# Kernel optimization log

Measured on AMD Instinct MI355X. Metric: run time of the kernel, lower is better.

## Reference

```python
import jax, jax.numpy as jnp
import numpy as np

N_ENTS = 50000
N_RELS = 500
EMB = 256
N_LAYERS = 2
N_EDGES = 400000
BATCH = 512
BN_EPS = 1e-5


def make_quaternion_mul(kernel):
    # kernel: [m, 4*dim] -> hamilton: [4*m, 4*dim]
    r, i, j, k = jnp.split(kernel, 4, axis=1)
    r2 = jnp.concatenate([r, -i, -j, -k], axis=0)
    i2 = jnp.concatenate([i, r, -k, j], axis=0)
    j2 = jnp.concatenate([j, k, r, -i], axis=0)
    k2 = jnp.concatenate([k, -j, i, r], axis=0)
    return jnp.concatenate([r2, i2, j2, k2], axis=1)


def batchnorm(x, gamma, beta):
    mean = jnp.mean(x, axis=0)
    var = jnp.var(x, axis=0)  # biased, as torch BN training normalization
    return (x - mean) * jax.lax.rsqrt(var + BN_EPS) * gamma + beta


def q4gnn_layer(X, rows, cols, vals, W, gamma, beta, n_nodes):
    hamilton = make_quaternion_mul(W)          # [d, d]
    support = X @ hamilton                     # [n, d]
    agg = jax.ops.segment_sum(vals[:, None] * support[cols], rows, num_segments=n_nodes)
    return jnp.tanh(batchnorm(agg, gamma, beta))


def vec_vec_wise_multiplication(q, p):
    # quaternion componentwise-normalized hamilton product; q, p: [B, d]
    d = q.shape[1]
    size = d // 4
    pn = p.reshape(-1, 4, size)
    pn = pn / jnp.sqrt(jnp.sum(pn * pn, axis=1, keepdims=True))
    pn = pn.reshape(-1, d)
    qr, qi, qj, qk = jnp.split(q, 4, axis=1)
    q_r = jnp.concatenate([qr, -qi, -qj, -qk], axis=1)
    q_i = jnp.concatenate([qi, qr, -qk, qj], axis=1)
    q_j = jnp.concatenate([qj, qk, qr, -qi], axis=1)
    q_k = jnp.concatenate([qk, -qj, qi, qr], axis=1)
    def qwise(x):
        return jnp.sum((x * pn).reshape(-1, 4, size), axis=1)
    return jnp.concatenate([qwise(q_r), qwise(q_i), qwise(q_j), qwise(q_k)], axis=1)


def quate_score(h, r, X, gamma, beta):
    hr = vec_vec_wise_multiplication(h, r)
    hr = batchnorm(hr, gamma, beta)            # dropout = identity (eval)
    return hr @ X.T                            # [B, n_ents]


def setup_inputs() -> dict:
    key = jax.random.key(0)
    ks = jax.random.split(key, 12)
    return {
        "e1_idx": jax.random.randint(ks[0], (BATCH,), 0, N_ENTS),
        "r_idx": jax.random.randint(ks[1], (BATCH,), 0, N_RELS),
        "embeddings": jax.random.normal(ks[2], (N_ENTS + N_RELS, EMB), jnp.float32) * 0.1,
        "gcn1_w": jax.random.normal(ks[3], (N_LAYERS, EMB // 4, EMB), jnp.float32) * 0.1,
        "gcn2_w": jax.random.normal(ks[4], (N_LAYERS, EMB // 4, EMB), jnp.float32) * 0.1,
        "gcn1_gamma": jnp.ones((N_LAYERS, EMB), jnp.float32),
        "gcn1_beta": jnp.zeros((N_LAYERS, EMB), jnp.float32),
        "gcn2_gamma": jnp.ones((N_LAYERS, EMB), jnp.float32),
        "gcn2_beta": jnp.zeros((N_LAYERS, EMB), jnp.float32),
        "lin_ents": jax.random.normal(ks[5], (N_LAYERS, EMB // 2, EMB), jnp.float32) * 0.1,
        "bn_s_gamma": jnp.ones((3, EMB), jnp.float32),
        "bn_s_beta": jnp.zeros((3, EMB), jnp.float32),
        "adj_rows": jax.random.randint(ks[6], (N_EDGES,), 0, N_ENTS),
        "adj_cols": jax.random.randint(ks[7], (N_EDGES,), 0, N_ENTS),
        "adj_vals": jax.random.uniform(ks[8], (N_EDGES,), jnp.float32),
        "adjr_rows": jax.random.randint(ks[9], (N_EDGES,), 0, N_ENTS + N_RELS),
        "adjr_cols": jax.random.randint(ks[10], (N_EDGES,), 0, N_ENTS + N_RELS),
        "adjr_vals": jax.random.uniform(ks[11], (N_EDGES,), jnp.float32),
    }


def reference(e1_idx, r_idx, embeddings, gcn1_w, gcn2_w, gcn1_gamma, gcn1_beta,
              gcn2_gamma, gcn2_beta, lin_ents, bn_s_gamma, bn_s_beta,
              adj_rows, adj_cols, adj_vals, adjr_rows, adjr_cols, adjr_vals):
    X = embeddings[:N_ENTS]
    R = embeddings[N_ENTS:]
    scores = [jax.nn.sigmoid(quate_score(X[e1_idx], R[r_idx], X, bn_s_gamma[0], bn_s_beta[0]))]
    for l in range(N_LAYERS):
        XR = jnp.concatenate([X, R], axis=0)
        XRrf = q4gnn_layer(XR, adjr_rows, adjr_cols, adjr_vals,
                           gcn2_w[l], gcn2_gamma[l], gcn2_beta[l], N_ENTS + N_RELS)
        Xef = q4gnn_layer(X, adj_rows, adj_cols, adj_vals,
                          gcn1_w[l], gcn1_gamma[l], gcn1_beta[l], N_ENTS)
        Xrf = XRrf[:N_ENTS]
        # combine_type == 'cat': interleave quaternion components -> [N, 2*EMB]
        e1, e2, e3, e4 = jnp.split(Xef, 4, axis=1)
        r1, r2, r3, r4 = jnp.split(Xrf, 4, axis=1)
        Xcat = jnp.concatenate([e1, r1, e2, r2, e3, r3, e4, r4], axis=1)
        X = Xcat @ make_quaternion_mul(lin_ents[l])  # [N, EMB]
        R = XRrf[N_ENTS:]
        scores.append(jax.nn.sigmoid(
            quate_score(X[e1_idx], R[r_idx], X, bn_s_gamma[l + 1], bn_s_beta[l + 1])))
    return jnp.stack(scores)  # [N_LAYERS+1, B, N_ENTS]
```

## Files before the change

### kernel.cpp

```cpp
#include <hip/hip_runtime.h>
#include <math.h>

#define N_ENTS 50000
#define N_RELS 500
#define N_ALL  50500
#define EMB    256
#define NEDGE  400000
#define BATCH  512
#define BN_EPS 1e-5f

typedef unsigned short u16;
typedef unsigned int   u32;
typedef __attribute__((ext_vector_type(8))) short s16x8;
typedef __attribute__((ext_vector_type(4))) float f32x4;

#define LSTR 40

__device__ __forceinline__ u16 f2b(float x) {
    u32 u = __float_as_uint(x);
    return (u16)((u + 0x7fffu + ((u >> 16) & 1u)) >> 16);
}
__device__ __forceinline__ float b2f(u16 h) {
    return __uint_as_float((u32)h << 16);
}

__global__ __launch_bounds__(256) void split_kernel(
    const float* __restrict__ x, u16* __restrict__ hi, u16* __restrict__ lo,
    long n4) {
    long i = (long)blockIdx.x * 256 + threadIdx.x;
    if (i >= n4) return;
    float4 v = ((const float4*)x)[i];
    u16 h0 = f2b(v.x), h1 = f2b(v.y), h2 = f2b(v.z), h3 = f2b(v.w);
    u16 l0 = f2b(v.x - b2f(h0)), l1 = f2b(v.y - b2f(h1));
    u16 l2 = f2b(v.z - b2f(h2)), l3 = f2b(v.w - b2f(h3));
    uint2 hp, lp;
    hp.x = (u32)h0 | ((u32)h1 << 16); hp.y = (u32)h2 | ((u32)h3 << 16);
    lp.x = (u32)l0 | ((u32)l1 << 16); lp.y = (u32)l2 | ((u32)l3 << 16);
    ((uint2*)hi)[i] = hp;
    ((uint2*)lo)[i] = lp;
}

__global__ __launch_bounds__(256) void build_ht_kernel(
    const float* __restrict__ W, u16* __restrict__ Hhi, u16* __restrict__ Hlo,
    int P) {
    int K4 = 4 * P;
    int idx = blockIdx.x * 256 + threadIdx.x;
    int total = 256 * K4;
    if (idx >= total) return;
    int n = idx / K4, k = idx - n * K4;
    int a = k / P, p = k - a * P;
    int c = n >> 6, s = n & 63;
    const int  comp[4][4] = {{0,1,2,3},{1,0,3,2},{2,3,0,1},{3,2,1,0}};
    const float sgn[4][4] = {{1.f,1.f,1.f,1.f},
                             {-1.f,1.f,1.f,-1.f},
                             {-1.f,-1.f,1.f,1.f},
                             {-1.f,1.f,-1.f,1.f}};
    float v = sgn[a][c] * W[p * 256 + comp[a][c] * 64 + s];
    u16 h = f2b(v);
    Hhi[idx] = h;
    Hlo[idx] = f2b(v - b2f(h));
}

template <int ROWS>
__device__ __forceinline__ void stage_rows(
    const u16* __restrict__ Shi, const u16* __restrict__ Slo,
    long row0, int rows_left, int K, int k0,
    u16* __restrict__ Lh, u16* __restrict__ Ll, int tid) {
#pragma unroll
    for (int p = 0; p < ROWS / 64; p++) {
        int idx = tid + p * 256;
        int r = idx >> 2, c = idx & 3;
        uint4 vh = make_uint4(0, 0, 0, 0), vl = make_uint4(0, 0, 0, 0);
        if (r < rows_left) {
            long base = (row0 + r) * (long)K + k0 + c * 8;
            vh = *(const uint4*)&Shi[base];
            vl = *(const uint4*)&Slo[base];
        }
        *(uint4*)&Lh[r * LSTR + c * 8] = vh;
        *(uint4*)&Ll[r * LSTR + c * 8] = vl;
    }
}

__device__ __forceinline__ void stage_f32_split(
    const float* __restrict__ S, long row0, int rows_left, int K, int k0,
    u16* __restrict__ Lh, u16* __restrict__ Ll, int tid) {
#pragma unroll
    for (int p = 0; p < 4; p++) {
        int idx = tid + p * 256;
        int r = idx >> 3, c4 = idx & 7;
        float4 v = make_float4(0.f, 0.f, 0.f, 0.f);
        if (r < rows_left)
            v = *(const float4*)&S[(row0 + r) * (long)K + k0 + c4 * 4];
        u16 h0 = f2b(v.x), h1 = f2b(v.y), h2 = f2b(v.z), h3 = f2b(v.w);
        u16 l0 = f2b(v.x - b2f(h0)), l1 = f2b(v.y - b2f(h1));
        u16 l2 = f2b(v.z - b2f(h2)), l3 = f2b(v.w - b2f(h3));
        uint2 hp, lp;
        hp.x = (u32)h0 | ((u32)h1 << 16); hp.y = (u32)h2 | ((u32)h3 << 16);
        lp.x = (u32)l0 | ((u32)l1 << 16); lp.y = (u32)l2 | ((u32)l3 << 16);
        *(uint2*)&Lh[r * LSTR + c4 * 4] = hp;
        *(uint2*)&Ll[r * LSTR + c4 * 4] = lp;
    }
}

__device__ __forceinline__ void mfma_tile256(
    const u16* __restrict__ Ah, const u16* __restrict__ Al,
    const u16* __restrict__ Bh, const u16* __restrict__ Bl,
    int wm, int wn, int lane, f32x4 acc[4][8]) {
    int lr = lane & 15, kg = lane >> 4;
    s16x8 ah[4], al[4];
#pragma unroll
    for (int fm = 0; fm < 4; fm++) {
        int off = (wm + fm * 16 + lr) * LSTR + kg * 8;
        ah[fm] = *(const s16x8*)&Ah[off];
        al[fm] = *(const s16x8*)&Al[off];
    }
#pragma unroll
    for (int fn = 0; fn < 8; fn++) {
        int off = (wn + fn * 16 + lr) * LSTR + kg * 8;
        s16x8 bh = *(const s16x8*)&Bh[off];
        s16x8 bl = *(const s16x8*)&Bl[off];
#pragma unroll
        for (int fm = 0; fm < 4; fm++) {
            acc[fm][fn] = __builtin_amdgcn_mfma_f32_16x16x32_bf16(
                ah[fm], bh, acc[fm][fn], 0, 0, 0);
            acc[fm][fn] = __builtin_amdgcn_mfma_f32_16x16x32_bf16(
                ah[fm], bl, acc[fm][fn], 0, 0, 0);
            acc[fm][fn] = __builtin_amdgcn_mfma_f32_16x16x32_bf16(
                al[fm], bh, acc[fm][fn], 0, 0, 0);
        }
    }
}

__global__ __launch_bounds__(256, 2) void mfma_agg_kernel(
    const float* __restrict__ G,
    const u16* __restrict__ Bhi, const u16* __restrict__ Blo,
    float* __restrict__ C, int M) {
    __shared__ u16 Ah[128 * LSTR], Al[128 * LSTR];
    __shared__ u16 Bh[256 * LSTR], Bl[256 * LSTR];
    int tid = threadIdx.x, lane = tid & 63, wid = tid >> 6;
    int wm = (wid >> 1) * 64, wn = (wid & 1) * 128;
    long bm0 = (long)blockIdx.y * 128;
    int rA = (int)(((long)M - bm0 < 128) ? (long)M - bm0 : 128);
    f32x4 acc[4][8] = {};
    for (int k0 = 0; k0 < 256; k0 += 32) {
        if (k0) __syncthreads();
        stage_f32_split(G, bm0, rA, 256, k0, Ah, Al, tid);
        stage_rows<256>(Bhi, Blo, 0, 256, 256, k0, Bh, Bl, tid);
        __syncthreads();
        mfma_tile256(Ah, Al, Bh, Bl, wm, wn, lane, acc);
    }
    int lr = lane & 15, lq = lane >> 4;
#pragma unroll
    for (int fm = 0; fm < 4; fm++) {
#pragma unroll
        for (int r = 0; r < 4; r++) {
            long row = bm0 + wm + fm * 16 + lq * 4 + r;
            if (row < M) {
#pragma unroll
                for (int fn = 0; fn < 8; fn++) {
                    long col = wn + fn * 16 + lr;
                    C[row * 256 + col] = acc[fm][fn][r];
                }
            }
        }
    }
}

__global__ __launch_bounds__(256, 2) void mfma_score_kernel(
    const u16* __restrict__ Ahi, const u16* __restrict__ Alo,
    const u16* __restrict__ Bhi, const u16* __restrict__ Blo,
    float* __restrict__ out) {
    __shared__ u16 Ah[128 * LSTR], Al[128 * LSTR];
    __shared__ u16 Bh[256 * LSTR], Bl[256 * LSTR];
    int tid = threadIdx.x, lane = tid & 63, wid = tid >> 6;
    int wm = (wid >> 1) * 64, wn = (wid & 1) * 128;
    long bm0 = (long)blockIdx.y * 128, bn0 = (long)blockIdx.x * 256;
    int rB = (int)(((long)N_ENTS - bn0 < 256) ? (long)N_ENTS - bn0 : 256);
    f32x4 acc[4][8] = {};
    for (int k0 = 0; k0 < 256; k0 += 32) {
        if (k0) __syncthreads();
        stage_rows<128>(Ahi, Alo, bm0, 128, 256, k0, Ah, Al, tid);
        stage_rows<256>(Bhi, Blo, bn0, rB, 256, k0, Bh, Bl, tid);
        __syncthreads();
        mfma_tile256(Ah, Al, Bh, Bl, wm, wn, lane, acc);
    }
    int lr = lane & 15, lq = lane >> 4;
#pragma unroll
    for (int fm = 0; fm < 4; fm++) {
#pragma unroll
        for (int r = 0; r < 4; r++) {
            long row = bm0 + wm + fm * 16 + lq * 4 + r;
#pragma unroll
            for (int fn = 0; fn < 8; fn++) {
                long col = bn0 + wn + fn * 16 + lr;
                if (col < N_ENTS) {
                    float v = acc[fm][fn][r];
                    out[row * N_ENTS + col] = 1.f / (1.f + __expf(-v));
                }
            }
        }
    }
}

__device__ __forceinline__ float4 lin_a_load(const float* __restrict__ Xef,
                                             const float* __restrict__ Xrf,
                                             int gm, int kk, int M) {
    int chunk = kk >> 6, s = kk & 63;
    const float* src = (chunk & 1) ? Xrf : Xef;
    float4 v = make_float4(0.f, 0.f, 0.f, 0.f);
    if (gm < M) v = *(const float4*)&src[(long)gm * 256 + (chunk >> 1) * 64 + s];
    return v;
}

__global__ __launch_bounds__(256, 2) void mfma_lin_kernel(
    const float* __restrict__ Xef, const float* __restrict__ Xrf,
    const u16* __restrict__ Bhi, const u16* __restrict__ Blo,
    u16* __restrict__ Chi, u16* __restrict__ Clo, int M) {
    __shared__ u16 Ah[128 * LSTR], Al[128 * LSTR];
    __shared__ u16 Bh[256 * LSTR], Bl[256 * LSTR];
    int tid = threadIdx.x, lane = tid & 63, wid = tid >> 6;
    int wm = (wid >> 1) * 64, wn = (wid & 1) * 128;
    int bm0 = blockIdx.y * 128;
    f32x4 acc[4][8] = {};
    for (int k0 = 0; k0 < 512; k0 += 32) {
        if (k0) __syncthreads();
#pragma unroll
        for (int p = 0; p < 4; p++) {
            int idx = tid + p * 256;
            int r = idx >> 3, c4 = idx & 7;
            float4 v = lin_a_load(Xef, Xrf, bm0 + r, k0 + c4 * 4, M);
            u16 h0 = f2b(v.x), h1 = f2b(v.y), h2 = f2b(v.z), h3 = f2b(v.w);
            u16 l0 = f2b(v.x - b2f(h0)), l1 = f2b(v.y - b2f(h1));
            u16 l2 = f2b(v.z - b2f(h2)), l3 = f2b(v.w - b2f(h3));
            uint2 hp, lp;
            hp.x = (u32)h0 | ((u32)h1 << 16); hp.y = (u32)h2 | ((u32)h3 << 16);
            lp.x = (u32)l0 | ((u32)l1 << 16); lp.y = (u32)l2 | ((u32)l3 << 16);
            *(uint2*)&Ah[r * LSTR + c4 * 4] = hp;
            *(uint2*)&Al[r * LSTR + c4 * 4] = lp;
        }
        stage_rows<256>(Bhi, Blo, 0, 256, 512, k0, Bh, Bl, tid);
        __syncthreads();
        mfma_tile256(Ah, Al, Bh, Bl, wm, wn, lane, acc);
    }
    int lr = lane & 15, lq = lane >> 4;
#pragma unroll
    for (int fm = 0; fm < 4; fm++) {
#pragma unroll
        for (int r = 0; r < 4; r++) {
            long row = (long)bm0 + wm + fm * 16 + lq * 4 + r;
            if (row < M) {
#pragma unroll
                for (int fn = 0; fn < 8; fn++) {
                    long col = wn + fn * 16 + lr;
                    float v = acc[fm][fn][r];
                    u16 h = f2b(v);
                    Chi[row * 256 + col] = h;
                    Clo[row * 256 + col] = f2b(v - b2f(h));
                }
            }
        }
    }
}

__global__ __launch_bounds__(256) void hist_kernel(
    const int* __restrict__ rows, int* __restrict__ cnt, int n_edges) {
    int e = blockIdx.x * 256 + threadIdx.x;
    if (e < n_edges) atomicAdd(&cnt[rows[e]], 1);
}

__global__ __launch_bounds__(1024) void exscan_kernel(
    const int* __restrict__ cnt, int n, int* __restrict__ off) {
    __shared__ int part[1024];
    int t = threadIdx.x;
    int chunk = (n + 1023) / 1024;
    int lo = t * chunk;
    int hi = lo + chunk; if (hi > n) hi = n;
    int s = 0;
    for (int i = lo; i < hi; i++) s += cnt[i];
    part[t] = s;
    __syncthreads();
    for (int d = 1; d < 1024; d <<= 1) {
        int v = (t >= d) ? part[t - d] : 0;
        __syncthreads();
        part[t] += v;
        __syncthreads();
    }
    int base = (t == 0) ? 0 : part[t - 1];
    for (int i = lo; i < hi; i++) {
        off[i] = base;
        base += cnt[i];
    }
    if (hi >= n) off[n] = base;
}

__global__ __launch_bounds__(256) void scatter_kernel(
    const int* __restrict__ rows, const int* __restrict__ cols,
    const float* __restrict__ vals, int* __restrict__ cursor,
    int2* __restrict__ pack, int n_edges) {
    int e = blockIdx.x * 256 + threadIdx.x;
    if (e >= n_edges) return;
    int r = rows[e];
    int p = atomicAdd(&cursor[r], 1);
    pack[p] = make_int2(cols[e], __float_as_int(vals[e]));
}

__global__ __launch_bounds__(256) void csr_gather_kernel(
    const u16* __restrict__ xhi, const u16* __restrict__ xlo,
    const int* __restrict__ off, const int2* __restrict__ pack,
    float* __restrict__ G, int n_rows) {
    int gid = blockIdx.x * 256 + threadIdx.x;
    int row = gid >> 6;
    int lane = gid & 63;
    if (row >= n_rows) return;
    int beg = off[row], end = off[row + 1];
    float4 acc = {0.f, 0.f, 0.f, 0.f};
    int e = beg;
    for (; e + 4 <= end; e += 4) {
        int2 cv0 = pack[e], cv1 = pack[e + 1], cv2 = pack[e + 2], cv3 = pack[e + 3];
        long b0 = (long)cv0.x * 256 + lane * 4;
        long b1 = (long)cv1.x * 256 + lane * 4;
        long b2 = (long)cv2.x * 256 + lane * 4;
        long b3 = (long)cv3.x * 256 + lane * 4;
        uint2 h0 = *(const uint2*)(xhi + b0), l0 = *(const uint2*)(xlo + b0);
        uint2 h1 = *(const uint2*)(xhi + b1), l1 = *(const uint2*)(xlo + b1);
        uint2 h2 = *(const uint2*)(xhi + b2), l2 = *(const uint2*)(xlo + b2);
        uint2 h3 = *(const uint2*)(xhi + b3), l3 = *(const uint2*)(xlo + b3);
        float v0 = __int_as_float(cv0.y), v1 = __int_as_float(cv1.y);
        float v2 = __int_as_float(cv2.y), v3 = __int_as_float(cv3.y);
        acc.x = fmaf(v0, b2f((u16)(h0.x & 0xffff)) + b2f((u16)(l0.x & 0xffff)), acc.x);
        acc.y = fmaf(v0, b2f((u16)(h0.x >> 16))    + b2f((u16)(l0.x >> 16)),    acc.y);
        acc.z = fmaf(v0, b2f((u16)(h0.y & 0xffff)) + b2f((u16)(l0.y & 0xffff)), acc.z);
        acc.w = fmaf(v0, b2f((u16)(h0.y >> 16))    + b2f((u16)(l0.y >> 16)),    acc.w);
        acc.x = fmaf(v1, b2f((u16)(h1.x & 0xffff)) + b2f((u16)(l1.x & 0xffff)), acc.x);
        acc.y = fmaf(v1, b2f((u16)(h1.x >> 16))    + b2f((u16)(l1.x >> 16)),    acc.y);
        acc.z = fmaf(v1, b2f((u16)(h1.y & 0xffff)) + b2f((u16)(l1.y & 0xffff)), acc.z);
        acc.w = fmaf(v1, b2f((u16)(h1.y >> 16))    + b2f((u16)(l1.y >> 16)),    acc.w);
        acc.x = fmaf(v2, b2f((u16)(h2.x & 0xffff)) + b2f((u16)(l2.x & 0xffff)), acc.x);
        acc.y = fmaf(v2, b2f((u16)(h2.x >> 16))    + b2f((u16)(l2.x >> 16)),    acc.y);
        acc.z = fmaf(v2, b2f((u16)(h2.y & 0xffff)) + b2f((u16)(l2.y & 0xffff)), acc.z);
        acc.w = fmaf(v2, b2f((u16)(h2.y >> 16))    + b2f((u16)(l2.y >> 16)),    acc.w);
        acc.x = fmaf(v3, b2f((u16)(h3.x & 0xffff)) + b2f((u16)(l3.x & 0xffff)), acc.x);
        acc.y = fmaf(v3, b2f((u16)(h3.x >> 16))    + b2f((u16)(l3.x >> 16)),    acc.y);
        acc.z = fmaf(v3, b2f((u16)(h3.y & 0xffff)) + b2f((u16)(l3.y & 0xffff)), acc.z);
        acc.w = fmaf(v3, b2f((u16)(h3.y >> 16))    + b2f((u16)(l3.y >> 16)),    acc.w);
    }
    for (; e < end; e++) {
        int2 cv = pack[e];
        float v = __int_as_float(cv.y);
        long b = (long)cv.x * 256 + lane * 4;
        uint2 hv = *(const uint2*)(xhi + b), lv = *(const uint2*)(xlo + b);
        acc.x = fmaf(v, b2f((u16)(hv.x & 0xffff)) + b2f((u16)(lv.x & 0xffff)), acc.x);
        acc.y = fmaf(v, b2f((u16)(hv.x >> 16))    + b2f((u16)(lv.x >> 16)),    acc.y);
        acc.z = fmaf(v, b2f((u16)(hv.y & 0xffff)) + b2f((u16)(lv.y & 0xffff)), acc.z);
        acc.w = fmaf(v, b2f((u16)(hv.y >> 16))    + b2f((u16)(lv.y >> 16)),    acc.w);
    }
    *(float4*)(G + (long)row * 256 + lane * 4) = acc;
}

__global__ __launch_bounds__(256) void bn_stats_kernel(
    const float* __restrict__ x, int n, float* __restrict__ stats) {
    int col = threadIdx.x;
    int r0 = blockIdx.x * 256;
    int r1 = r0 + 256;
    if (r1 > n) r1 = n;
    float s = 0.f, sq = 0.f;
    for (int r = r0; r < r1; r++) {
        float v = x[(long)r * 256 + col];
        s += v;
        sq += v * v;
    }
    atomicAdd(&stats[col], s);
    atomicAdd(&stats[256 + col], sq);
}

template <bool TANH>
__global__ __launch_bounds__(256) void bn_apply_kernel(
    const float* __restrict__ x, float* __restrict__ y, int n,
    const float* __restrict__ gamma, const float* __restrict__ beta,
    const float* __restrict__ stats) {
    long total = (long)n * 256;
    float inv_n = 1.f / (float)n;
    for (long idx = (long)blockIdx.x * 256 + threadIdx.x; idx < total;
         idx += (long)gridDim.x * 256) {
        int col = (int)(idx & 255);
        float mean = stats[col] * inv_n;
        float var = stats[256 + col] * inv_n - mean * mean;
        float sc = rsqrtf(var + BN_EPS) * gamma[col];
        float v = (x[idx] - mean) * sc + beta[col];
        if (TANH) v = tanhf(v);
        y[idx] = v;
    }
}

__global__ __launch_bounds__(256) void bn_apply_split_kernel(
    const float* __restrict__ x, u16* __restrict__ hi, u16* __restrict__ lo,
    int n, const float* __restrict__ gamma, const float* __restrict__ beta,
    const float* __restrict__ stats) {
    long total = (long)n * 256;
    float inv_n = 1.f / (float)n;
    long idx = (long)blockIdx.x * 256 + threadIdx.x;
    if (idx >= total) return;
    int col = (int)(idx & 255);
    float mean = stats[col] * inv_n;
    float var = stats[256 + col] * inv_n - mean * mean;
    float sc = rsqrtf(var + BN_EPS) * gamma[col];
    float v = (x[idx] - mean) * sc + beta[col];
    u16 h = f2b(v);
    hi[idx] = h;
    lo[idx] = f2b(v - b2f(h));
}

__global__ __launch_bounds__(256) void hr_kernel(
    const u16* __restrict__ xhi, const u16* __restrict__ xlo,
    const int* __restrict__ e1_idx, const int* __restrict__ r_idx,
    float* __restrict__ hr) {
    int idx = blockIdx.x * 256 + threadIdx.x;
    if (idx >= BATCH * 64) return;
    int b = idx >> 6, s = idx & 63;
    long hrow = (long)e1_idx[b] * 256;
    long prow = ((long)N_ENTS + r_idx[b]) * 256;
    float qr = b2f(xhi[hrow + s])       + b2f(xlo[hrow + s]);
    float qi = b2f(xhi[hrow + 64 + s])  + b2f(xlo[hrow + 64 + s]);
    float qj = b2f(xhi[hrow + 128 + s]) + b2f(xlo[hrow + 128 + s]);
    float qk = b2f(xhi[hrow + 192 + s]) + b2f(xlo[hrow + 192 + s]);
    float pr = b2f(xhi[prow + s])       + b2f(xlo[prow + s]);
    float pi = b2f(xhi[prow + 64 + s])  + b2f(xlo[prow + 64 + s]);
    float pj = b2f(xhi[prow + 128 + s]) + b2f(xlo[prow + 128 + s]);
    float pk = b2f(xhi[prow + 192 + s]) + b2f(xlo[prow + 192 + s]);
    float inv = rsqrtf(pr * pr + pi * pi + pj * pj + pk * pk);
    pr *= inv; pi *= inv; pj *= inv; pk *= inv;
    float* o = hr + (long)b * 256 + s;
    o[0]   = qr * pr - qi * pi - qj * pj - qk * pk;
    o[64]  = qi * pr + qr * pi - qk * pj + qj * pk;
    o[128] = qj * pr + qk * pi + qr * pj - qi * pk;
    o[192] = qk * pr - qj * pi + qi * pj + qr * pk;
}

struct Csr {
    int* off;
    int* cur;
    int2* pack;
};

struct Ws {
    float* Gbuf;
    float* aggA;
    float* aggB;
    float* hr;
    float* stats;
    u16* xr_hi;
    u16* xr_lo;
    u16* hrn_hi;
    u16* hrn_lo;
    u16* ht_hi;
    u16* ht_lo;
    Csr adj;
    Csr adjr;
};

static void build_csr(const int* rows, const int* cols, const float* vals,
                      int n_rows, const Csr& c, hipStream_t stream) {
    hipMemsetAsync(c.cur, 0, (size_t)n_rows * sizeof(int), stream);
    hist_kernel<<<(NEDGE + 255) / 256, 256, 0, stream>>>(rows, c.cur, NEDGE);
    exscan_kernel<<<1, 1024, 0, stream>>>(c.cur, n_rows, c.off);
    hipMemcpyAsync(c.cur, c.off, (size_t)n_rows * sizeof(int),
                   hipMemcpyDeviceToDevice, stream);
    scatter_kernel<<<(NEDGE + 255) / 256, 256, 0, stream>>>(
        rows, cols, vals, c.cur, c.pack, NEDGE);
}

static void run_bn(float* buf, float* outbuf, int n, const float* gamma,
                   const float* beta, bool do_tanh, const Ws& w,
                   hipStream_t stream) {
    hipMemsetAsync(w.stats, 0, 512 * sizeof(float), stream);
    bn_stats_kernel<<<(n + 255) / 256, 256, 0, stream>>>(buf, n, w.stats);
    long total = (long)n * 256;
    int blocks = (int)((total + 255) / 256);
    if (blocks > 2048) blocks = 2048;
    if (do_tanh)
        bn_apply_kernel<true><<<blocks, 256, 0, stream>>>(buf, outbuf, n, gamma, beta, w.stats);
    else
        bn_apply_kernel<false><<<blocks, 256, 0, stream>>>(buf, outbuf, n, gamma, beta, w.stats);
}

static void run_split(const float* x, u16* hi, u16* lo, long n,
                      hipStream_t stream) {
    long n4 = n / 4;
    split_kernel<<<(int)((n4 + 255) / 256), 256, 0, stream>>>(x, hi, lo, n4);
}

static void run_q4gnn(int n, const Csr& c, const float* W, const float* gamma,
                      const float* beta, float* agg, const Ws& w,
                      hipStream_t stream) {
    int gblocks = (n * 64 + 255) / 256;
    csr_gather_kernel<<<gblocks, 256, 0, stream>>>(
        w.xr_hi, w.xr_lo, c.off, c.pack, w.Gbuf, n);
    build_ht_kernel<<<(256 * 256) / 256, 256, 0, stream>>>(W, w.ht_hi, w.ht_lo, 64);
    dim3 g(1, (n + 127) / 128);
    mfma_agg_kernel<<<g, 256, 0, stream>>>(w.Gbuf, w.ht_hi, w.ht_lo, agg, n);
    run_bn(agg, agg, n, gamma, beta, true, w, stream);
}

static void run_score(const int* e1_idx, const int* r_idx, const float* gamma,
                      const float* beta, float* out_l, const Ws& w,
                      hipStream_t stream) {
    hr_kernel<<<(BATCH * 64) / 256, 256, 0, stream>>>(
        w.xr_hi, w.xr_lo, e1_idx, r_idx, w.hr);
    hipMemsetAsync(w.stats, 0, 512 * sizeof(float), stream);
    bn_stats_kernel<<<(BATCH + 255) / 256, 256, 0, stream>>>(w.hr, BATCH, w.stats);
    bn_apply_split_kernel<<<(BATCH * 256) / 256, 256, 0, stream>>>(
        w.hr, w.hrn_hi, w.hrn_lo, BATCH, gamma, beta, w.stats);
    dim3 g((N_ENTS + 255) / 256, BATCH / 128);
    mfma_score_kernel<<<g, 256, 0, stream>>>(
        w.hrn_hi, w.hrn_lo, w.xr_hi, w.xr_lo, out_l);
}

extern "C" void kernel_launch(void* const* d_in, const int* in_sizes, int n_in,
                              void* d_out, int out_size, void* d_ws, size_t ws_size,
                              hipStream_t stream) {
    const int*   e1_idx     = (const int*)d_in[0];
    const int*   r_idx      = (const int*)d_in[1];
    const float* emb        = (const float*)d_in[2];
    const float* gcn1_w     = (const float*)d_in[3];
    const float* gcn2_w     = (const float*)d_in[4];
    const float* gcn1_gamma = (const float*)d_in[5];
    const float* gcn1_beta  = (const float*)d_in[6];
    const float* gcn2_gamma = (const float*)d_in[7];
    const float* gcn2_beta  = (const float*)d_in[8];
    const float* lin_ents   = (const float*)d_in[9];
    const float* bn_s_gamma = (const float*)d_in[10];
    const float* bn_s_beta  = (const float*)d_in[11];
    const int*   adj_rows   = (const int*)d_in[12];
    const int*   adj_cols   = (const int*)d_in[13];
    const float* adj_vals   = (const float*)d_in[14];
    const int*   adjr_rows  = (const int*)d_in[15];
    const int*   adjr_cols  = (const int*)d_in[16];
    const float* adjr_vals  = (const float*)d_in[17];
    float* out = (float*)d_out;

    Ws w;
    float* f = (float*)d_ws;
    w.Gbuf       = f; f += (long)N_ALL * EMB;
    w.aggA       = f; f += (long)N_ALL * EMB;
    w.aggB       = f; f += (long)N_ENTS * EMB;
    w.hr         = f; f += BATCH * EMB;
    w.stats      = f; f += 512;
    w.xr_hi  = (u16*)f; f += (long)N_ALL * EMB / 2;
    w.xr_lo  = (u16*)f; f += (long)N_ALL * EMB / 2;
    w.hrn_hi = (u16*)f; f += BATCH * EMB / 2;
    w.hrn_lo = (u16*)f; f += BATCH * EMB / 2;
    w.ht_hi  = (u16*)f; f += 256 * 512 / 2;
    w.ht_lo  = (u16*)f; f += 256 * 512 / 2;
    int* ip = (int*)f;
    w.adj.pack  = (int2*)ip; ip += 2 * NEDGE;
    w.adjr.pack = (int2*)ip; ip += 2 * NEDGE;
    w.adj.off    = ip; ip += N_ENTS + 1;
    w.adj.cur    = ip; ip += N_ENTS;
    w.adjr.off   = ip; ip += N_ALL + 1;
    w.adjr.cur   = ip; ip += N_ALL;

    build_csr(adj_rows, adj_cols, adj_vals, N_ENTS, w.adj, stream);
    build_csr(adjr_rows, adjr_cols, adjr_vals, N_ALL, w.adjr, stream);

    run_split(emb, w.xr_hi, w.xr_lo, (long)N_ALL * EMB, stream);

    run_score(e1_idx, r_idx, bn_s_gamma, bn_s_beta, out, w, stream);

    for (int l = 0; l < 2; l++) {
        run_q4gnn(N_ALL, w.adjr, gcn2_w + (long)l * 64 * 256,
                  gcn2_gamma + l * 256, gcn2_beta + l * 256, w.aggA, w, stream);
        run_q4gnn(N_ENTS, w.adj, gcn1_w + (long)l * 64 * 256,
                  gcn1_gamma + l * 256, gcn1_beta + l * 256, w.aggB, w, stream);
        build_ht_kernel<<<(256 * 512) / 256, 256, 0, stream>>>(
            lin_ents + (long)l * 128 * 256, w.ht_hi, w.ht_lo, 128);
        dim3 g(1, (N_ENTS + 127) / 128);
        mfma_lin_kernel<<<g, 256, 0, stream>>>(
            w.aggB, w.aggA, w.ht_hi, w.ht_lo, w.xr_hi, w.xr_lo, N_ENTS);
        run_split(w.aggA + (long)N_ENTS * EMB, w.xr_hi + (long)N_ENTS * EMB,
                  w.xr_lo + (long)N_ENTS * EMB, (long)N_RELS * EMB, stream);
        run_score(e1_idx, r_idx, bn_s_gamma + (l + 1) * 256,
                  bn_s_beta + (l + 1) * 256,
                  out + (long)(l + 1) * BATCH * N_ENTS, w, stream);
    }
}
```

Before: 1.889 ms.

## Fuse BN statistics into aggregation GEMM and BN+tanh into linear prologue

The aggregation MFMA kernel now accumulates per-column sum and sum-of-squares with wave shuffles and atomics, which removes the separate BN stats pass over the aggregate. A tiny kernel turns the stats into scale and shift coefficients. BN and tanh are then applied while the linear GEMM loads its A tiles, and a small fused kernel does the same for the relation rows, which removes the separate full-size bn_apply read and write passes. The cost is extra tanh work inside the lin kernel's staging loop and atomic contention on 512 stats addresses.

```diff
diff --git a/kernel.cpp b/kernel.cpp
--- a/kernel.cpp
+++ b/kernel.cpp
@@ -61,6 +61,17 @@
     Hlo[idx] = f2b(v - b2f(h));
 }
 
+__global__ __launch_bounds__(256) void bn_coeff_kernel(
+    const float* __restrict__ stats, int n, const float* __restrict__ gamma,
+    const float* __restrict__ beta, float2* __restrict__ coef) {
+    int col = threadIdx.x;
+    float inv_n = 1.f / (float)n;
+    float mean = stats[col] * inv_n;
+    float var = stats[256 + col] * inv_n - mean * mean;
+    float sc = rsqrtf(var + BN_EPS) * gamma[col];
+    coef[col] = make_float2(sc, beta[col] - mean * sc);
+}
+
 template <int ROWS>
 __device__ __forceinline__ void stage_rows(
     const u16* __restrict__ Shi, const u16* __restrict__ Slo,
@@ -134,7 +145,7 @@
 __global__ __launch_bounds__(256, 2) void mfma_agg_kernel(
     const float* __restrict__ G,
     const u16* __restrict__ Bhi, const u16* __restrict__ Blo,
-    float* __restrict__ C, int M) {
+    float* __restrict__ C, float* __restrict__ stats, int M) {
     __shared__ u16 Ah[128 * LSTR], Al[128 * LSTR];
     __shared__ u16 Bh[256 * LSTR], Bl[256 * LSTR];
     int tid = threadIdx.x, lane = tid & 63, wid = tid >> 6;
@@ -162,6 +173,25 @@
                     C[row * 256 + col] = acc[fm][fn][r];
                 }
             }
+        }
+    }
+#pragma unroll
+    for (int fn = 0; fn < 8; fn++) {
+        float s = 0.f, sq = 0.f;
+#pragma unroll
+        for (int fm = 0; fm < 4; fm++)
+#pragma unroll
+            for (int r = 0; r < 4; r++) {
+                float v = acc[fm][fn][r];
+                s += v;
+                sq += v * v;
+            }
+        s += __shfl_xor(s, 16);  s += __shfl_xor(s, 32);
+        sq += __shfl_xor(sq, 16); sq += __shfl_xor(sq, 32);
+        if (lane < 16) {
+            int col = wn + fn * 16 + lr;
+            atomicAdd(&stats[col], s);
+            atomicAdd(&stats[256 + col], sq);
         }
     }
 }
@@ -202,18 +232,9 @@
     }
 }
 
-__device__ __forceinline__ float4 lin_a_load(const float* __restrict__ Xef,
-                                             const float* __restrict__ Xrf,
-                                             int gm, int kk, int M) {
-    int chunk = kk >> 6, s = kk & 63;
-    const float* src = (chunk & 1) ? Xrf : Xef;
-    float4 v = make_float4(0.f, 0.f, 0.f, 0.f);
-    if (gm < M) v = *(const float4*)&src[(long)gm * 256 + (chunk >> 1) * 64 + s];
-    return v;
-}
-
 __global__ __launch_bounds__(256, 2) void mfma_lin_kernel(
     const float* __restrict__ Xef, const float* __restrict__ Xrf,
+    const float2* __restrict__ coefE, const float2* __restrict__ coefR,
     const u16* __restrict__ Bhi, const u16* __restrict__ Blo,
     u16* __restrict__ Chi, u16* __restrict__ Clo, int M) {
     __shared__ u16 Ah[128 * LSTR], Al[128 * LSTR];
@@ -228,7 +249,20 @@
         for (int p = 0; p < 4; p++) {
             int idx = tid + p * 256;
             int r = idx >> 3, c4 = idx & 7;
-            float4 v = lin_a_load(Xef, Xrf, bm0 + r, k0 + c4 * 4, M);
+            int kk = k0 + c4 * 4;
+            int chunk = kk >> 6, s = kk & 63;
+            int gm = bm0 + r;
+            const float* src = (chunk & 1) ? Xrf : Xef;
+            const float2* cf = (chunk & 1) ? coefR : coefE;
+            int base = (chunk >> 1) * 64 + s;
+            float4 v = make_float4(0.f, 0.f, 0.f, 0.f);
+            if (gm < M) v = *(const float4*)&src[(long)gm * 256 + base];
+            float2 c0 = cf[base], c1 = cf[base + 1];
+            float2 c2 = cf[base + 2], c3 = cf[base + 3];
+            v.x = tanhf(fmaf(v.x, c0.x, c0.y));
+            v.y = tanhf(fmaf(v.y, c1.x, c1.y));
+            v.z = tanhf(fmaf(v.z, c2.x, c2.y));
+            v.w = tanhf(fmaf(v.w, c3.x, c3.y));
             u16 h0 = f2b(v.x), h1 = f2b(v.y), h2 = f2b(v.z), h3 = f2b(v.w);
             u16 l0 = f2b(v.x - b2f(h0)), l1 = f2b(v.y - b2f(h1));
             u16 l2 = f2b(v.z - b2f(h2)), l3 = f2b(v.w - b2f(h3));
@@ -373,25 +407,6 @@
     atomicAdd(&stats[256 + col], sq);
 }
 
-template <bool TANH>
-__global__ __launch_bounds__(256) void bn_apply_kernel(
-    const float* __restrict__ x, float* __restrict__ y, int n,
-    const float* __restrict__ gamma, const float* __restrict__ beta,
-    const float* __restrict__ stats) {
-    long total = (long)n * 256;
-    float inv_n = 1.f / (float)n;
-    for (long idx = (long)blockIdx.x * 256 + threadIdx.x; idx < total;
-         idx += (long)gridDim.x * 256) {
-        int col = (int)(idx & 255);
-        float mean = stats[col] * inv_n;
-        float var = stats[256 + col] * inv_n - mean * mean;
-        float sc = rsqrtf(var + BN_EPS) * gamma[col];
-        float v = (x[idx] - mean) * sc + beta[col];
-        if (TANH) v = tanhf(v);
-        y[idx] = v;
-    }
-}
-
 __global__ __launch_bounds__(256) void bn_apply_split_kernel(
     const float* __restrict__ x, u16* __restrict__ hi, u16* __restrict__ lo,
     int n, const float* __restrict__ gamma, const float* __restrict__ beta,
@@ -405,6 +420,19 @@
     float var = stats[256 + col] * inv_n - mean * mean;
     float sc = rsqrtf(var + BN_EPS) * gamma[col];
     float v = (x[idx] - mean) * sc + beta[col];
+    u16 h = f2b(v);
+    hi[idx] = h;
+    lo[idx] = f2b(v - b2f(h));
+}
+
+__global__ __launch_bounds__(256) void bn_tanh_split_kernel(
+    const float* __restrict__ x, const float2* __restrict__ coef,
+    u16* __restrict__ hi, u16* __restrict__ lo, long total) {
+    long idx = (long)blockIdx.x * 256 + threadIdx.x;
+    if (idx >= total) return;
+    int col = (int)(idx & 255);
+    float2 c = coef[col];
+    float v = tanhf(fmaf(x[idx], c.x, c.y));
     u16 h = f2b(v);
     hi[idx] = h;
     lo[idx] = f2b(v - b2f(h));
@@ -447,7 +475,11 @@
     float* aggA;
     float* aggB;
     float* hr;
-    float* stats;
+    float* statsHr;
+    float* statsA;
+    float* statsB;
+    float2* coefA;
+    float2* coefB;
     u16* xr_hi;
     u16* xr_lo;
     u16* hrn_hi;
@@ -469,36 +501,24 @@
         rows, cols, vals, c.cur, c.pack, NEDGE);
 }
 
-static void run_bn(float* buf, float* outbuf, int n, const float* gamma,
-                   const float* beta, bool do_tanh, const Ws& w,
-                   hipStream_t stream) {
-    hipMemsetAsync(w.stats, 0, 512 * sizeof(float), stream);
-    bn_stats_kernel<<<(n + 255) / 256, 256, 0, stream>>>(buf, n, w.stats);
-    long total = (long)n * 256;
-    int blocks = (int)((total + 255) / 256);
-    if (blocks > 2048) blocks = 2048;
-    if (do_tanh)
-        bn_apply_kernel<true><<<blocks, 256, 0, stream>>>(buf, outbuf, n, gamma, beta, w.stats);
-    else
-        bn_apply_kernel<false><<<blocks, 256, 0, stream>>>(buf, outbuf, n, gamma, beta, w.stats);
-}
-
 static void run_split(const float* x, u16* hi, u16* lo, long n,
                       hipStream_t stream) {
     long n4 = n / 4;
     split_kernel<<<(int)((n4 + 255) / 256), 256, 0, stream>>>(x, hi, lo, n4);
 }
 
-static void run_q4gnn(int n, const Csr& c, const float* W, const float* gamma,
-                      const float* beta, float* agg, const Ws& w,
-                      hipStream_t stream) {
+static void run_q4gnn(int n, const Csr& c, const float* W,
+                      const float* gamma, const float* beta,
+                      float* agg, float* stats, float2* coef,
+                      const Ws& w, hipStream_t stream) {
+    hipMemsetAsync(stats, 0, 512 * sizeof(float), stream);
     int gblocks = (n * 64 + 255) / 256;
     csr_gather_kernel<<<gblocks, 256, 0, stream>>>(
         w.xr_hi, w.xr_lo, c.off, c.pack, w.Gbuf, n);
     build_ht_kernel<<<(256 * 256) / 256, 256, 0, stream>>>(W, w.ht_hi, w.ht_lo, 64);
     dim3 g(1, (n + 127) / 128);
-    mfma_agg_kernel<<<g, 256, 0, stream>>>(w.Gbuf, w.ht_hi, w.ht_lo, agg, n);
-    run_bn(agg, agg, n, gamma, beta, true, w, stream);
+    mfma_agg_kernel<<<g, 256, 0, stream>>>(w.Gbuf, w.ht_hi, w.ht_lo, agg, stats, n);
+    bn_coeff_kernel<<<1, 256, 0, stream>>>(stats, n, gamma, beta, coef);
 }
 
 static void run_score(const int* e1_idx, const int* r_idx, const float* gamma,
@@ -506,10 +526,10 @@
                       hipStream_t stream) {
     hr_kernel<<<(BATCH * 64) / 256, 256, 0, stream>>>(
         w.xr_hi, w.xr_lo, e1_idx, r_idx, w.hr);
-    hipMemsetAsync(w.stats, 0, 512 * sizeof(float), stream);
-    bn_stats_kernel<<<(BATCH + 255) / 256, 256, 0, stream>>>(w.hr, BATCH, w.stats);
+    hipMemsetAsync(w.statsHr, 0, 512 * sizeof(float), stream);
+    bn_stats_kernel<<<(BATCH + 255) / 256, 256, 0, stream>>>(w.hr, BATCH, w.statsHr);
     bn_apply_split_kernel<<<(BATCH * 256) / 256, 256, 0, stream>>>(
-        w.hr, w.hrn_hi, w.hrn_lo, BATCH, gamma, beta, w.stats);
+        w.hr, w.hrn_hi, w.hrn_lo, BATCH, gamma, beta, w.statsHr);
     dim3 g((N_ENTS + 255) / 256, BATCH / 128);
     mfma_score_kernel<<<g, 256, 0, stream>>>(
         w.hrn_hi, w.hrn_lo, w.xr_hi, w.xr_lo, out_l);
@@ -544,7 +564,11 @@
     w.aggA       = f; f += (long)N_ALL * EMB;
     w.aggB       = f; f += (long)N_ENTS * EMB;
     w.hr         = f; f += BATCH * EMB;
-    w.stats      = f; f += 512;
+    w.statsHr    = f; f += 512;
+    w.statsA     = f; f += 512;
+    w.statsB     = f; f += 512;
+    w.coefA      = (float2*)f; f += 512;
+    w.coefB      = (float2*)f; f += 512;
     w.xr_hi  = (u16*)f; f += (long)N_ALL * EMB / 2;
     w.xr_lo  = (u16*)f; f += (long)N_ALL * EMB / 2;
     w.hrn_hi = (u16*)f; f += BATCH * EMB / 2;
@@ -568,16 +592,21 @@
 
     for (int l = 0; l < 2; l++) {
         run_q4gnn(N_ALL, w.adjr, gcn2_w + (long)l * 64 * 256,
-                  gcn2_gamma + l * 256, gcn2_beta + l * 256, w.aggA, w, stream);
+                  gcn2_gamma + l * 256, gcn2_beta + l * 256,
+                  w.aggA, w.statsA, w.coefA, w, stream);
         run_q4gnn(N_ENTS, w.adj, gcn1_w + (long)l * 64 * 256,
-                  gcn1_gamma + l * 256, gcn1_beta + l * 256, w.aggB, w, stream);
+                  gcn1_gamma + l * 256, gcn1_beta + l * 256,
+                  w.aggB, w.statsB, w.coefB, w, stream);
         build_ht_kernel<<<(256 * 512) / 256, 256, 0, stream>>>(
             lin_ents + (long)l * 128 * 256, w.ht_hi, w.ht_lo, 128);
         dim3 g(1, (N_ENTS + 127) / 128);
         mfma_lin_kernel<<<g, 256, 0, stream>>>(
-            w.aggB, w.aggA, w.ht_hi, w.ht_lo, w.xr_hi, w.xr_lo, N_ENTS);
-        run_split(w.aggA + (long)N_ENTS * EMB, w.xr_hi + (long)N_ENTS * EMB,
-                  w.xr_lo + (long)N_ENTS * EMB, (long)N_RELS * EMB, stream);
+            w.aggB, w.aggA, w.coefB, w.coefA, w.ht_hi, w.ht_lo,
+            w.xr_hi, w.xr_lo, N_ENTS);
+        bn_tanh_split_kernel<<<(N_RELS * EMB + 255) / 256, 256, 0, stream>>>(
+            w.aggA + (long)N_ENTS * EMB, w.coefA,
+            w.xr_hi + (long)N_ENTS * EMB, w.xr_lo + (long)N_ENTS * EMB,
+            (long)N_RELS * EMB);
         run_score(e1_idx, r_idx, bn_s_gamma + (l + 1) * 256,
                   bn_s_beta + (l + 1) * 256,
                   out + (long)(l + 1) * BATCH * N_ENTS, w, stream);
```

New measurement: 1.667 ms. -11.7%, faster.
